# Kernel tuning notes

Hardware: AMD Instinct MI355X
Metric: run time of the kernel (lower is better)

## Reference

```python
import jax, jax.numpy as jnp
import numpy as np
from jax import lax

# quantization bit widths (config)
IB, WB, RB, AB = 8, 4, 4, 8


def quantize(x, bw):
    """Signed fixed-point quantization to bw bits in [-1, 1) with STE."""
    scale = 2.0 ** (bw - 1)
    q = jnp.clip(jnp.round(x * scale), -scale, scale - 1) / scale
    return x + lax.stop_gradient(q - x)


def setup_inputs() -> dict:
    key = jax.random.key(0)
    k1, k2, k3, k4, k5 = jax.random.split(key, 5)
    B, T, I, H, O = 256, 1024, 64, 256, 16
    inputs = jax.random.normal(k1, (B, T, I), dtype=jnp.float32)
    # input kernel init: uniform(-1, 1)
    Wi = jax.random.uniform(k2, (H, I), dtype=jnp.float32, minval=-1.0, maxval=1.0)
    # recurrent kernel: orthogonal (geotorch parametrization); materialize via QR
    A = jax.random.normal(k3, (H, H), dtype=jnp.float32)
    Wr, _ = jnp.linalg.qr(A)
    Wr = Wr.astype(jnp.float32)
    Wo = jax.random.normal(k4, (O, H), dtype=jnp.float32) * 0.1
    b = jax.random.normal(k5, (H,), dtype=jnp.float32) * 0.01
    return {"inputs": inputs, "Wi": Wi, "Wr": Wr, "Wo": Wo, "b": b}


def reference(inputs, Wi, Wr, Wo, b):
    # quantize inputs (ib bits)
    x = quantize(inputs, IB)
    # quantized input projection, precomputed for all timesteps: [B,T,H]
    u = jnp.einsum("bti,hi->bth", x, quantize(Wi, WB))
    Wrq = quantize(Wr, RB)  # quantized orthogonal recurrent weight [H,H]
    B = inputs.shape[0]
    H = Wr.shape[0]
    h0 = jnp.zeros((B, H), dtype=inputs.dtype)

    def step(h, u_t):
        z = u_t + h @ Wrq.T                      # [B,H]
        m = jax.nn.relu(jnp.abs(z) + b)          # modrelu magnitude
        h_new = quantize(jnp.sign(z) * m, AB)    # quantized activation
        return h_new, None

    u_t = jnp.swapaxes(u, 0, 1)  # [T,B,H]
    h_last, _ = lax.scan(step, h0, u_t)
    # output head on last hidden state
    out = h_last @ quantize(Wo, WB).T  # [B,O]
    return out
```

## Files before the change

kernel.cpp:

```cpp
#include <hip/hip_runtime.h>


#define TSEQ 1024
#define IDIM 64
#define HDIM 256
#define ODIM 16

typedef int v4i __attribute__((ext_vector_type(4)));

__device__ __forceinline__ int sdot4i8(int a, int b, int c) {
#if __has_builtin(__builtin_amdgcn_sdot4)
    return __builtin_amdgcn_sdot4(a, b, c, false);
#else
    int r = c;
    r += ((a << 24) >> 24) * ((b << 24) >> 24);
    r += ((a << 16) >> 24) * ((b << 16) >> 24);
    r += ((a << 8)  >> 24) * ((b << 8)  >> 24);
    r += (a >> 24) * (b >> 24);
    return r;
#endif
}

__device__ __forceinline__ int qpack4(float4 f, float s, float lo, float hi) {
    int a = (int)fminf(fmaxf(rintf(f.x * s), lo), hi);
    int b = (int)fminf(fmaxf(rintf(f.y * s), lo), hi);
    int c = (int)fminf(fmaxf(rintf(f.z * s), lo), hi);
    int d = (int)fminf(fmaxf(rintf(f.w * s), lo), hi);
    return (a & 255) | ((b & 255) << 8) | ((c & 255) << 16) | ((d & 255) << 24);
}

__global__ __launch_bounds__(256, 1)
void qornn_kernel(const float* __restrict__ x, const float* __restrict__ Wi,
                  const float* __restrict__ Wr, const float* __restrict__ Wo,
                  const float* __restrict__ bias, float* __restrict__ out) {
    __shared__ alignas(16) int xlds[TSEQ * 16 + 16];
    __shared__ alignas(16) int wstage[8192];
    __shared__ alignas(16) int wo_lds[1024];
    __shared__ alignas(16) int hbuf[2][64];

    const int tid = threadIdx.x;
    const int brow = blockIdx.x;
    const int w = tid >> 6;
    const int l = tid & 63;
    const int g = l >> 4;
    const int n = l & 15;

    {
        const float4* wi4 = (const float4*)Wi;
        #pragma unroll
        for (int it = 0; it < 16; ++it) {
            int flat = it * 256 + tid;
            wstage[flat] = qpack4(wi4[flat], 8.0f, -8.0f, 7.0f);
        }
    }
    __syncthreads();
    v4i wiB[4];
    #pragma unroll
    for (int t4 = 0; t4 < 4; ++t4)
        wiB[t4] = *(const v4i*)(wstage + (w * 64 + t4 * 16 + n) * 16 + g * 4);
    __syncthreads();

    v4i wrB[16];
    {
        const float4* wr4 = (const float4*)Wr;
        #pragma unroll
        for (int half = 0; half < 2; ++half) {
            #pragma unroll
            for (int it = 0; it < 32; ++it) {
                int flat = it * 256 + tid;
                wstage[flat] = qpack4(wr4[half * 8192 + flat], 8.0f, -8.0f, 7.0f);
            }
            __syncthreads();
            if ((w >> 1) == half) {
                const int rl = (w & 1) * 64;
                #pragma unroll
                for (int t4 = 0; t4 < 4; ++t4)
                    #pragma unroll
                    for (int j = 0; j < 4; ++j)
                        wrB[t4 * 4 + j] =
                            *(const v4i*)(wstage + (rl + t4 * 16 + n) * 64 + j * 16 + g * 4);
            }
            __syncthreads();
        }
    }

    {
        const float4* wo4 = (const float4*)Wo;
        #pragma unroll
        for (int it = 0; it < 4; ++it) {
            int flat = it * 256 + tid;
            wo_lds[flat] = qpack4(wo4[flat], 8.0f, -8.0f, 7.0f);
        }
    }

    {
        const float4* rowf4 = (const float4*)(x + (size_t)brow * (TSEQ * IDIM));
        #pragma unroll 8
        for (int it = 0; it < 64; ++it) {
            int flat = it * 256 + tid;
            xlds[flat] = qpack4(rowf4[flat], 128.0f, -128.0f, 127.0f);
        }
    }
    if (tid < 64) hbuf[0][tid] = 0;
    __syncthreads();

    const float bv128 = bias[tid] * 128.0f;
    const v4i zero4 = {0, 0, 0, 0};

    v4i accp[4];
    {
        const v4i xA = *(const v4i*)(xlds + g * 4);
        #pragma unroll
        for (int t4 = 0; t4 < 4; ++t4)
            accp[t4] = __builtin_amdgcn_mfma_i32_16x16x64_i8(xA, wiB[t4], zero4, 0, 0, 0);
    }

    #pragma unroll 2
    for (int t = 0; t < TSEQ; ++t) {
        const char* hsrc = (const char*)hbuf[t & 1];
        v4i hA[4];
        #pragma unroll
        for (int j = 0; j < 4; ++j)
            hA[j] = *(const v4i*)(hsrc + j * 64 + g * 16);

        v4i acc[4];
        #pragma unroll
        for (int t4 = 0; t4 < 4; ++t4) {
            acc[t4] = accp[t4];
            #pragma unroll
            for (int j = 0; j < 4; ++j)
                acc[t4] = __builtin_amdgcn_mfma_i32_16x16x64_i8(hA[j], wrB[t4 * 4 + j],
                                                                acc[t4], 0, 0, 0);
        }

        const int zz = (g == 0) ? acc[0].x : (g == 1) ? acc[1].x
                     : (g == 2) ? acc[2].x : acc[3].x;

        const float zf = (float)zz;
        const float t1 = fmaf(fabsf(zf), 0.125f, bv128);
        const float t2 = fmaxf(t1, 0.0f);
        const float r  = rintf(t2);
        const int vpos = (int)fminf(r, 127.0f);
        const int vneg = -(int)fminf(r, 128.0f);
        int hv = (zz < 0) ? vneg : vpos;
        hv = (zz == 0) ? 0 : hv;

        ((signed char*)hbuf[(t + 1) & 1])[tid] = (signed char)hv;

        const v4i xA = *(const v4i*)(xlds + (t + 1) * 16 + g * 4);
        #pragma unroll
        for (int t4 = 0; t4 < 4; ++t4)
            accp[t4] = __builtin_amdgcn_mfma_i32_16x16x64_i8(xA, wiB[t4], zero4, 0, 0, 0);

        __syncthreads();
    }

    if (tid < ODIM) {
        const int4* wo = (const int4*)wo_lds;
        const int4* hl = (const int4*)hbuf[0];
        int a0 = 0, a1 = 0, a2 = 0, a3 = 0;
        #pragma unroll
        for (int i = 0; i < 16; ++i) {
            int4 w4 = wo[tid * 16 + i];
            int4 h4 = hl[i];
            a0 = sdot4i8(h4.x, w4.x, a0);
            a1 = sdot4i8(h4.y, w4.y, a1);
            a2 = sdot4i8(h4.z, w4.z, a2);
            a3 = sdot4i8(h4.w, w4.w, a3);
        }
        out[brow * ODIM + tid] = (float)((a0 + a1) + (a2 + a3)) * 0.0009765625f;
    }
}

extern "C" void kernel_launch(void* const* d_in, const int* in_sizes, int n_in,
                              void* d_out, int out_size, void* d_ws, size_t ws_size,
                              hipStream_t stream) {
    const float* x  = (const float*)d_in[0];
    const float* Wi = (const float*)d_in[1];
    const float* Wr = (const float*)d_in[2];
    const float* Wo = (const float*)d_in[3];
    const float* b  = (const float*)d_in[4];
    float* out = (float*)d_out;

    const int B = in_sizes[0] / (TSEQ * IDIM);
    qornn_kernel<<<B, HDIM, 0, stream>>>(x, Wi, Wr, Wo, b, out);
}
```

Before: 428.3 us.

## Split recurrent matvec between MFMA and VALU sdot4 with lane shuffles

Each wave now computes half of its hidden-unit tiles with MFMA and the other half with VALU sdot4 dot products reduced by cross-lane xor shuffles. The input projection is split the same way. The goal is to shorten the serial MFMA dependency chain on each timestep by running matrix and vector units in parallel. The cost is extra VALU instructions, shuffles and register pressure on the per-step critical path.

After: 454.6 us. 6.1% more time.

```diff
diff --git a/kernel.cpp b/kernel.cpp
--- a/kernel.cpp
+++ b/kernel.cpp
@@ -54,13 +54,17 @@
         }
     }
     __syncthreads();
-    v4i wiB[4];
+    v4i wiB[2], wiV[2];
     #pragma unroll
-    for (int t4 = 0; t4 < 4; ++t4)
+    for (int t4 = 0; t4 < 2; ++t4)
         wiB[t4] = *(const v4i*)(wstage + (w * 64 + t4 * 16 + n) * 16 + g * 4);
+    #pragma unroll
+    for (int i = 0; i < 2; ++i)
+        wiV[i] = *(const v4i*)(wstage + (w * 64 + 32 + i * 16 + n) * 16 + g * 4);
     __syncthreads();
 
-    v4i wrB[16];
+    v4i wrB[2][4];
+    v4i wrV[2][4];
     {
         const float4* wr4 = (const float4*)Wr;
         #pragma unroll
@@ -74,11 +78,17 @@
             if ((w >> 1) == half) {
                 const int rl = (w & 1) * 64;
                 #pragma unroll
-                for (int t4 = 0; t4 < 4; ++t4)
+                for (int t4 = 0; t4 < 2; ++t4)
                     #pragma unroll
                     for (int j = 0; j < 4; ++j)
-                        wrB[t4 * 4 + j] =
+                        wrB[t4][j] =
                             *(const v4i*)(wstage + (rl + t4 * 16 + n) * 64 + j * 16 + g * 4);
+                #pragma unroll
+                for (int i = 0; i < 2; ++i)
+                    #pragma unroll
+                    for (int j = 0; j < 4; ++j)
+                        wrV[i][j] =
+                            *(const v4i*)(wstage + (rl + 32 + i * 16 + n) * 64 + j * 16 + g * 4);
             }
             __syncthreads();
         }
@@ -107,12 +117,20 @@
     const float bv128 = bias[tid] * 128.0f;
     const v4i zero4 = {0, 0, 0, 0};
 
-    v4i accp[4];
-    {
-        const v4i xA = *(const v4i*)(xlds + g * 4);
-        #pragma unroll
-        for (int t4 = 0; t4 < 4; ++t4)
-            accp[t4] = __builtin_amdgcn_mfma_i32_16x16x64_i8(xA, wiB[t4], zero4, 0, 0, 0);
+    v4i accp0, accp1;
+    int uV0, uV1;
+    {
+        const v4i xA = *(const v4i*)((const char*)xlds + g * 16);
+        accp0 = __builtin_amdgcn_mfma_i32_16x16x64_i8(xA, wiB[0], zero4, 0, 0, 0);
+        accp1 = __builtin_amdgcn_mfma_i32_16x16x64_i8(xA, wiB[1], zero4, 0, 0, 0);
+        int s0 = sdot4i8(xA.x, wiV[0].x, 0);
+        s0 = sdot4i8(xA.y, wiV[0].y, s0);
+        s0 = sdot4i8(xA.z, wiV[0].z, s0);
+        uV0 = sdot4i8(xA.w, wiV[0].w, s0);
+        int s1 = sdot4i8(xA.x, wiV[1].x, 0);
+        s1 = sdot4i8(xA.y, wiV[1].y, s1);
+        s1 = sdot4i8(xA.z, wiV[1].z, s1);
+        uV1 = sdot4i8(xA.w, wiV[1].w, s1);
     }
 
     #pragma unroll 2
@@ -123,18 +141,46 @@
         for (int j = 0; j < 4; ++j)
             hA[j] = *(const v4i*)(hsrc + j * 64 + g * 16);
 
-        v4i acc[4];
-        #pragma unroll
-        for (int t4 = 0; t4 < 4; ++t4) {
-            acc[t4] = accp[t4];
-            #pragma unroll
-            for (int j = 0; j < 4; ++j)
-                acc[t4] = __builtin_amdgcn_mfma_i32_16x16x64_i8(hA[j], wrB[t4 * 4 + j],
-                                                                acc[t4], 0, 0, 0);
-        }
-
-        const int zz = (g == 0) ? acc[0].x : (g == 1) ? acc[1].x
-                     : (g == 2) ? acc[2].x : acc[3].x;
+        v4i acc0 = accp0, acc1 = accp1;
+        #pragma unroll
+        for (int j = 0; j < 4; ++j) {
+            acc0 = __builtin_amdgcn_mfma_i32_16x16x64_i8(hA[j], wrB[0][j], acc0, 0, 0, 0);
+            acc1 = __builtin_amdgcn_mfma_i32_16x16x64_i8(hA[j], wrB[1][j], acc1, 0, 0, 0);
+        }
+
+        int p0a = uV0, p0b = 0, p1a = uV1, p1b = 0;
+        #pragma unroll
+        for (int j = 0; j < 2; ++j) {
+            p0a = sdot4i8(hA[j].x, wrV[0][j].x, p0a);
+            p0a = sdot4i8(hA[j].y, wrV[0][j].y, p0a);
+            p0a = sdot4i8(hA[j].z, wrV[0][j].z, p0a);
+            p0a = sdot4i8(hA[j].w, wrV[0][j].w, p0a);
+            p1a = sdot4i8(hA[j].x, wrV[1][j].x, p1a);
+            p1a = sdot4i8(hA[j].y, wrV[1][j].y, p1a);
+            p1a = sdot4i8(hA[j].z, wrV[1][j].z, p1a);
+            p1a = sdot4i8(hA[j].w, wrV[1][j].w, p1a);
+        }
+        #pragma unroll
+        for (int j = 2; j < 4; ++j) {
+            p0b = sdot4i8(hA[j].x, wrV[0][j].x, p0b);
+            p0b = sdot4i8(hA[j].y, wrV[0][j].y, p0b);
+            p0b = sdot4i8(hA[j].z, wrV[0][j].z, p0b);
+            p0b = sdot4i8(hA[j].w, wrV[0][j].w, p0b);
+            p1b = sdot4i8(hA[j].x, wrV[1][j].x, p1b);
+            p1b = sdot4i8(hA[j].y, wrV[1][j].y, p1b);
+            p1b = sdot4i8(hA[j].z, wrV[1][j].z, p1b);
+            p1b = sdot4i8(hA[j].w, wrV[1][j].w, p1b);
+        }
+        int p0 = p0a + p0b;
+        int p1 = p1a + p1b;
+        p0 += __shfl_xor(p0, 16);
+        p1 += __shfl_xor(p1, 16);
+        p0 += __shfl_xor(p0, 32);
+        p1 += __shfl_xor(p1, 32);
+
+        const int zmf = (g == 0) ? acc0.x : acc1.x;
+        const int zvl = (g == 2) ? p0 : p1;
+        const int zz  = (g < 2) ? zmf : zvl;
 
         const float zf = (float)zz;
         const float t1 = fmaf(fabsf(zf), 0.125f, bv128);
@@ -147,10 +193,17 @@
 
         ((signed char*)hbuf[(t + 1) & 1])[tid] = (signed char)hv;
 
-        const v4i xA = *(const v4i*)(xlds + (t + 1) * 16 + g * 4);
-        #pragma unroll
-        for (int t4 = 0; t4 < 4; ++t4)
-            accp[t4] = __builtin_amdgcn_mfma_i32_16x16x64_i8(xA, wiB[t4], zero4, 0, 0, 0);
+        const v4i xA = *(const v4i*)((const char*)xlds + (t + 1) * 64 + g * 16);
+        accp0 = __builtin_amdgcn_mfma_i32_16x16x64_i8(xA, wiB[0], zero4, 0, 0, 0);
+        accp1 = __builtin_amdgcn_mfma_i32_16x16x64_i8(xA, wiB[1], zero4, 0, 0, 0);
+        int s0 = sdot4i8(xA.x, wiV[0].x, 0);
+        s0 = sdot4i8(xA.y, wiV[0].y, s0);
+        s0 = sdot4i8(xA.z, wiV[0].z, s0);
+        uV0 = sdot4i8(xA.w, wiV[0].w, s0);
+        int s1 = sdot4i8(xA.x, wiV[1].x, 0);
+        s1 = sdot4i8(xA.y, wiV[1].y, s1);
+        s1 = sdot4i8(xA.z, wiV[1].z, s1);
+        uV1 = sdot4i8(xA.w, wiV[1].w, s1);
 
         __syncthreads();
     }
```
